# Kernel tuning notes

Measured on AMD Instinct MI355X. Metric: run time of the kernel, lower is better.

The kernel has to match this reference:

```python
import jax, jax.numpy as jnp
import numpy as np

N_NODES = 100000
N_EDGES = 1_600_000


def _glorot(key, shape):
    fan_in, fan_out = shape
    s = jnp.sqrt(6.0 / (fan_in + fan_out)).astype(jnp.float32)
    return jax.random.uniform(key, shape, jnp.float32, -1.0, 1.0) * s


def setup_inputs() -> dict:
    key = jax.random.key(0)
    ks = jax.random.split(key, 6)
    x = jax.random.normal(ks[0], (N_NODES, 88), jnp.float32)
    edge_index = jax.random.randint(ks[1], (2, N_EDGES), 0, N_NODES, dtype=jnp.int32)
    return {
        "x": x,
        "W1": _glorot(ks[2], (88, 65)), "b1": jnp.zeros((65,), jnp.float32),
        "W2": _glorot(ks[3], (65, 50)), "b2": jnp.zeros((50,), jnp.float32),
        "W3": _glorot(ks[4], (50, 65)), "b3": jnp.zeros((65,), jnp.float32),
        "W4": _glorot(ks[5], (65, 88)), "b4": jnp.zeros((88,), jnp.float32),
        "edge_index": edge_index,
    }


def _gcn_conv(h, W, b, src, dst, norm, n):
    # PyG GCNConv: transform, then normalized neighbor aggregation (self-loops
    # already folded into src/dst/norm).
    h = h @ W                                  # [N, out]
    msg = h[src] * norm[:, None]               # [E+N, out] gather
    return jax.ops.segment_sum(msg, dst, num_segments=n) + b  # scatter-add


def reference(x, W1, b1, W2, b2, W3, b3, W4, b4, edge_index):
    n = x.shape[0]
    loop = jnp.arange(n, dtype=edge_index.dtype)
    src = jnp.concatenate([edge_index[0], loop])   # add self-loops
    dst = jnp.concatenate([edge_index[1], loop])
    deg = jax.ops.segment_sum(jnp.ones_like(dst, dtype=x.dtype), dst, num_segments=n)
    dinv = jnp.where(deg > 0, jax.lax.rsqrt(deg), 0.0)
    norm = dinv[src] * dinv[dst]                   # D^-1/2 (A+I) D^-1/2 edge weights

    # encoder
    h = jax.nn.relu(_gcn_conv(x, W1, b1, src, dst, norm, n))
    h = _gcn_conv(h, W2, b2, src, dst, norm, n)
    # decoder
    h = jax.nn.relu(_gcn_conv(h, W3, b3, src, dst, norm, n))
    return _gcn_conv(h, W4, b4, src, dst, norm, n)
```

## Files before the change

kernel.cpp:

```cpp
#include <hip/hip_runtime.h>

#define BS 256
#define FB 1024
#define NB 256
#define CHUNK 4096
#define CAP 64
#define LCAP 8192

using half8 = __attribute__((ext_vector_type(8))) _Float16;

template<typename T>
__device__ __forceinline__ void load8f(const T* p, float (&d)[8]) {
    if constexpr (sizeof(T) == 4) {
        float4 a = *(const float4*)p;
        float4 b = *(const float4*)(p + 4);
        d[0] = a.x; d[1] = a.y; d[2] = a.z; d[3] = a.w;
        d[4] = b.x; d[5] = b.y; d[6] = b.z; d[7] = b.w;
    } else {
        half8 v = *(const half8*)p;
        #pragma unroll
        for (int j = 0; j < 8; ++j) d[j] = (float)v[j];
    }
}
template<typename T>
__device__ __forceinline__ void store8f(T* p, const float (&d)[8]) {
    if constexpr (sizeof(T) == 4) {
        *(float4*)p       = make_float4(d[0], d[1], d[2], d[3]);
        *(float4*)(p + 4) = make_float4(d[4], d[5], d[6], d[7]);
    } else {
        half8 h;
        #pragma unroll
        for (int j = 0; j < 8; ++j) h[j] = (_Float16)d[j];
        *(half8*)p = h;
    }
}


__global__ __launch_bounds__(BS) void k_zero1(int* a, int n) {
    int i = blockIdx.x * BS + threadIdx.x;
    if (i < n) a[i] = 0;
}

__global__ __launch_bounds__(BS) void k_bucket(const int* __restrict__ src, const int* __restrict__ dst,
                                               unsigned* __restrict__ bbuf, int* __restrict__ bcounts,
                                               int E, unsigned long long invB, int bsz) {
    __shared__ int lcnt[NB];
    for (int t = threadIdx.x; t < NB; t += BS) lcnt[t] = 0;
    __syncthreads();
    int base_e = blockIdx.x * CHUNK;
    unsigned* mybuf = bbuf + (size_t)blockIdx.x * NB * CAP;
    #pragma unroll
    for (int j = 0; j < CHUNK / BS; ++j) {
        int e = base_e + j * BS + threadIdx.x;
        if (e < E) {
            int d = dst[e];
            int s = src[e];
            int b = (int)(((unsigned long long)(unsigned)d * invB) >> 40);
            int doff = d - b * bsz;
            int pos = atomicAdd(&lcnt[b], 1);
            if (pos < CAP)
                mybuf[b * CAP + pos] = ((unsigned)doff << 17) | (unsigned)s;
        }
    }
    __syncthreads();
    for (int t = threadIdx.x; t < NB; t += BS)
        bcounts[blockIdx.x * NB + t] = min(lcnt[t], CAP);
}

__global__ __launch_bounds__(FB) void k_cnt(const unsigned* __restrict__ bbuf, const int* __restrict__ bcounts,
                                            int* __restrict__ cnt, int nch, int bsz, int N) {
    __shared__ int lhist[512];
    for (int t = threadIdx.x; t < 512; t += FB) lhist[t] = 0;
    __syncthreads();
    int b = blockIdx.x;
    int lo = b * bsz;
    int total = nch * CAP;
    for (int idx = threadIdx.x; idx < total; idx += FB) {
        int seg = idx >> 6, slot = idx & 63;
        int c = bcounts[seg * NB + b];
        if (slot < c)
            atomicAdd(&lhist[bbuf[((size_t)seg * NB + b) * CAP + slot] >> 17], 1);
    }
    __syncthreads();
    int hi = min(N, lo + bsz);
    for (int t = threadIdx.x; t < hi - lo; t += FB) cnt[lo + t] = lhist[t];
}

__global__ __launch_bounds__(BS) void k_dinv(const int* __restrict__ cnt, float* __restrict__ dinv, int N) {
    int i = blockIdx.x * BS + threadIdx.x;
    if (i < N) dinv[i] = rsqrtf((float)(cnt[i] + 1));
}

__global__ __launch_bounds__(BS) void k_scan1(const int* __restrict__ cnt, int* __restrict__ bsum, int N) {
    __shared__ int s[BS];
    int i = blockIdx.x * BS + threadIdx.x;
    s[threadIdx.x] = (i < N) ? cnt[i] : 0;
    __syncthreads();
    for (int off = BS / 2; off > 0; off >>= 1) {
        if (threadIdx.x < off) s[threadIdx.x] += s[threadIdx.x + off];
        __syncthreads();
    }
    if (threadIdx.x == 0) bsum[blockIdx.x] = s[0];
}

__global__ __launch_bounds__(512) void k_scan2(int* bsum, int nb) {
    __shared__ int s[512];
    int t = threadIdx.x;
    int v = (t < nb) ? bsum[t] : 0;
    s[t] = v;
    __syncthreads();
    for (int off = 1; off < 512; off <<= 1) {
        int u = (t >= off) ? s[t - off] : 0;
        __syncthreads();
        s[t] += u;
        __syncthreads();
    }
    if (t < nb) bsum[t] = s[t] - v;
}

__global__ __launch_bounds__(BS) void k_scan3(const int* __restrict__ cnt, const int* __restrict__ boff,
                                              int* __restrict__ row_ptr, int N) {
    __shared__ int s[BS];
    int t = threadIdx.x;
    int i = blockIdx.x * BS + t;
    int v = (i < N) ? cnt[i] : 0;
    s[t] = v;
    __syncthreads();
    for (int off = 1; off < BS; off <<= 1) {
        int u = (t >= off) ? s[t - off] : 0;
        __syncthreads();
        s[t] += u;
        __syncthreads();
    }
    int base = boff[blockIdx.x];
    if (i < N) row_ptr[i] = base + s[t] - v;
    if (i == N - 1) row_ptr[N] = base + s[t];
}

__global__ __launch_bounds__(FB) void k_fill2(const unsigned* __restrict__ bbuf, const int* __restrict__ bcounts,
                                              const int* __restrict__ row_ptr, const float* __restrict__ dinv,
                                              uint2* __restrict__ entries,
                                              int nch, int bsz, int N) {
    __shared__ int cur[512];
    __shared__ float ldinv[512];
    __shared__ unsigned sorted[LCAP];

    int b = blockIdx.x;
    int lo = b * bsz;
    int hi = min(N, lo + bsz);
    int gbase = row_ptr[lo];
    int tot = row_ptr[hi] - gbase;
    for (int t = threadIdx.x; t < hi - lo; t += FB) {
        cur[t] = row_ptr[lo + t] - gbase;
        ldinv[t] = dinv[lo + t];
    }
    __syncthreads();

    int total = nch * CAP;
    for (int idx = threadIdx.x; idx < total; idx += FB) {
        int seg = idx >> 6, slot = idx & 63;
        int c = bcounts[seg * NB + b];
        if (slot < c) {
            unsigned u = bbuf[((size_t)seg * NB + b) * CAP + slot];
            int p = atomicAdd(&cur[u >> 17], 1);
            if (p < LCAP) sorted[p] = u;
        }
    }
    __syncthreads();

    for (int t = threadIdx.x; t < tot; t += FB) {
        unsigned u = sorted[t];
        int s = (int)(u & 0x1FFFFu);
        int doff = (int)(u >> 17);
        float w = dinv[s] * ldinv[doff];
        entries[gbase + t] = make_uint2((unsigned)s, __float_as_uint(w));
    }
}

template<typename TIN, int K, int M, int LDIN, int LDOUT, bool BIAS, bool RELU, typename TOUT>
__global__ __launch_bounds__(BS) void k_gemm(const TIN* __restrict__ H, const float* __restrict__ Wg,
                                             const float* __restrict__ bias, TOUT* __restrict__ out, int N) {
    constexpr int M8 = (M + 7) & ~7;
    constexpr int MS = M8 + 4;
    constexpr int CG = M8 / 8;
    __shared__ float Wl[K * MS];
    for (int idx = threadIdx.x; idx < K * MS; idx += BS) {
        int k = idx / MS, m = idx - k * MS;
        Wl[idx] = (m < M) ? Wg[(size_t)k * M + m] : 0.f;
    }
    __syncthreads();

    int nrb = (N + 1) >> 1;
    int idx = blockIdx.x * BS + threadIdx.x;
    if (idx >= nrb * CG) return;
    int rb = idx / CG;
    int cg = idx - rb * CG;
    int c0 = cg * 8;
    int r0 = rb * 2;
    bool two = (r0 + 1 < N);
    int r1 = two ? r0 + 1 : r0;
    const TIN* h0 = H + (size_t)r0 * LDIN;
    const TIN* h1 = H + (size_t)r1 * LDIN;

    float acc0[8], acc1[8];
    #pragma unroll
    for (int m = 0; m < 8; ++m) { acc0[m] = 0.f; acc1[m] = 0.f; }

    constexpr int K8 = K & ~7;
    #pragma unroll 1
    for (int k = 0; k < K8; k += 8) {
        float p0[8], p1[8];
        load8f(h0 + k, p0);
        load8f(h1 + k, p1);
        #pragma unroll
        for (int j = 0; j < 8; ++j) {
            const float* wl = &Wl[(k + j) * MS + c0];
            float4 wa = *(const float4*)wl;
            float4 wb = *(const float4*)(wl + 4);
            const float wv[8] = {wa.x, wa.y, wa.z, wa.w, wb.x, wb.y, wb.z, wb.w};
            #pragma unroll
            for (int m = 0; m < 8; ++m) {
                acc0[m] = fmaf(p0[j], wv[m], acc0[m]);
                acc1[m] = fmaf(p1[j], wv[m], acc1[m]);
            }
        }
    }
    #pragma unroll
    for (int k = K8; k < K; ++k) {
        float pa = (float)h0[k];
        float pb = (float)h1[k];
        const float* wl = &Wl[k * MS + c0];
        float4 wa = *(const float4*)wl;
        float4 wb = *(const float4*)(wl + 4);
        const float wv[8] = {wa.x, wa.y, wa.z, wa.w, wb.x, wb.y, wb.z, wb.w};
        #pragma unroll
        for (int m = 0; m < 8; ++m) {
            acc0[m] = fmaf(pa, wv[m], acc0[m]);
            acc1[m] = fmaf(pb, wv[m], acc1[m]);
        }
    }

    #pragma unroll
    for (int m = 0; m < 8; ++m) {
        int c = c0 + m;
        bool in = (c < M);
        float v0 = in ? acc0[m] : 0.f;
        float v1 = in ? acc1[m] : 0.f;
        if (BIAS && in) { float bb = bias[c]; v0 += bb; v1 += bb; }
        if (RELU) { v0 = fmaxf(v0, 0.f); v1 = fmaxf(v1, 0.f); }
        acc0[m] = v0; acc1[m] = v1;
    }
    store8f(out + (size_t)r0 * LDOUT + c0, acc0);
    if (two) store8f(out + (size_t)r1 * LDOUT + c0, acc1);
}

template<typename TIN, typename TOUT, int M, int M8, int LDI, int LDO, bool BIAS, bool RELU>
__global__ __launch_bounds__(BS) void k_agg(const TIN* __restrict__ T, TOUT* __restrict__ out,
                                            const int* __restrict__ row_ptr, const uint2* __restrict__ entries,
                                            const float* __restrict__ dinv, const float* __restrict__ bias,
                                            int N) {
    constexpr int CG = M8 / 8;
    int idx = blockIdx.x * BS + threadIdx.x;
    if (idx >= N * CG) return;
    int i  = idx / CG;
    int cg = idx - i * CG;
    int c0 = cg * 8;

    float di = dinv[i];
    float w0 = di * di;
    float t0[8];
    load8f(T + (size_t)i * LDI + c0, t0);
    float a0[8], a1[8];
    #pragma unroll
    for (int m = 0; m < 8; ++m) { a0[m] = w0 * t0[m]; a1[m] = 0.f; }

    int e0 = row_ptr[i], e1 = row_ptr[i + 1];
    for (int e = e0; e < e1; e += 8) {
        unsigned sidx[8];
        float w[8];
        #pragma unroll
        for (int j = 0; j < 8; ++j) {
            int ee = e + j;
            int ec = (ee < e1) ? ee : (e1 - 1);
            uint2 u = entries[ec];
            sidx[j] = u.x;
            w[j] = (ee < e1) ? __uint_as_float(u.y) : 0.f;
        }
        #pragma unroll
        for (int j = 0; j < 8; ++j) {
            float g[8];
            load8f(T + (size_t)sidx[j] * LDI + c0, g);
            if (j & 1) {
                #pragma unroll
                for (int m = 0; m < 8; ++m) a1[m] = fmaf(w[j], g[m], a1[m]);
            } else {
                #pragma unroll
                for (int m = 0; m < 8; ++m) a0[m] = fmaf(w[j], g[m], a0[m]);
            }
        }
    }

    #pragma unroll
    for (int m = 0; m < 8; ++m) {
        float v = a0[m] + a1[m];
        if (BIAS && (c0 + m) < M) v += bias[c0 + m];
        if (RELU) v = fmaxf(v, 0.f);
        a0[m] = v;
    }
    store8f(out + (size_t)i * LDO + c0, a0);
}


extern "C" void kernel_launch(void* const* d_in, const int* in_sizes, int n_in,
                              void* d_out, int out_size, void* d_ws, size_t ws_size,
                              hipStream_t stream) {
    const float* x  = (const float*)d_in[0];
    const float* W1 = (const float*)d_in[1];
    const float* b1 = (const float*)d_in[2];
    const float* W2 = (const float*)d_in[3];
    const float* b2 = (const float*)d_in[4];
    const float* W3 = (const float*)d_in[5];
    const float* b3 = (const float*)d_in[6];
    const float* W4 = (const float*)d_in[7];
    const float* b4 = (const float*)d_in[8];
    const int* edge_index = (const int*)d_in[9];

    const int N = in_sizes[0] / 88;
    const int E = in_sizes[9] / 2;
    const int* src = edge_index;
    const int* dst = edge_index + E;

    const int nch = (E + CHUNK - 1) / CHUNK;
    const int bsz = (N + NB - 1) / NB;
    const unsigned long long invB = ((1ull << 40) + bsz - 1) / bsz;

    auto al = [](size_t b) { return (b + 255) & ~(size_t)255; };
    char* p = (char*)d_ws;
    auto carve = [&](size_t bytes) { void* r = p; p += (bytes + 255) & ~(size_t)255; return r; };
    int*   cnt     = (int*)  carve((size_t)N * 4);
    float* dinv    = (float*)carve((size_t)N * 4);
    int*   row_ptr = (int*)  carve((size_t)(N + 1) * 4);
    int*   bsum    = (int*)  carve(4096);
    uint2* entries = (uint2*)carve((size_t)E * 8);

    char* ub = p;
    int*      bcounts = (int*)ub;
    unsigned* bbuf    = (unsigned*)(ub + al((size_t)nch * NB * 4));
    size_t csr_bytes  = al((size_t)nch * NB * 4) + al((size_t)nch * NB * CAP * 4);

    size_t hbytes = al((size_t)N * 72 * 2);
    _Float16* hA = (_Float16*)ub;
    _Float16* hB = (_Float16*)(ub + hbytes);
    _Float16* hC = (_Float16*)(ub + 2 * hbytes);
    size_t h_bytes_tot = 3 * hbytes;

    p = ub + (csr_bytes > h_bytes_tot ? csr_bytes : h_bytes_tot);
    (void)p; (void)ws_size;

    int gN = (N + BS - 1) / BS;

    k_zero1 <<<gN, BS, 0, stream>>>(cnt, N);
    k_bucket<<<nch, BS, 0, stream>>>(src, dst, bbuf, bcounts, E, invB, bsz);
    k_cnt   <<<NB, FB, 0, stream>>>(bbuf, bcounts, cnt, nch, bsz, N);
    k_dinv  <<<gN, BS, 0, stream>>>(cnt, dinv, N);
    k_scan1 <<<gN, BS, 0, stream>>>(cnt, bsum, N);
    k_scan2 <<<1, 512, 0, stream>>>(bsum, gN);
    k_scan3 <<<gN, BS, 0, stream>>>(cnt, bsum, row_ptr, N);
    k_fill2 <<<NB, FB, 0, stream>>>(bbuf, bcounts, row_ptr, dinv, entries, nch, bsz, N);

    auto agg_grid  = [&](int CG) { return (N * CG + BS - 1) / BS; };
    auto gemm_grid = [&](int M)  { int M8 = (M + 7) & ~7; int CG = M8 / 8;
                                   return (((N + 1) / 2) * CG + BS - 1) / BS; };

    k_gemm<float, 88, 65, 88, 72, false, false, _Float16><<<gemm_grid(65), BS, 0, stream>>>(x, W1, nullptr, hA, N);
    k_agg<_Float16, _Float16, 65, 72, 72, 72, true, true><<<agg_grid(9), BS, 0, stream>>>(hA, hB, row_ptr, entries, dinv, b1, N);
    k_gemm<_Float16, 65, 50, 72, 56, false, false, _Float16><<<gemm_grid(50), BS, 0, stream>>>(hB, W2, nullptr, hC, N);
    k_agg<_Float16, _Float16, 50, 56, 56, 56, true, false><<<agg_grid(7), BS, 0, stream>>>(hC, hA, row_ptr, entries, dinv, b2, N);
    k_agg<_Float16, _Float16, 50, 56, 56, 56, false, false><<<agg_grid(7), BS, 0, stream>>>(hA, hB, row_ptr, entries, dinv, nullptr, N);
    k_gemm<_Float16, 50, 65, 56, 72, true, true, _Float16><<<gemm_grid(65), BS, 0, stream>>>(hB, W3, b3, hC, N);
    k_agg<_Float16, _Float16, 65, 72, 72, 72, false, false><<<agg_grid(9), BS, 0, stream>>>(hC, hA, row_ptr, entries, dinv, nullptr, N);
    k_gemm<_Float16, 65, 88, 72, 88, true, false, float><<<gemm_grid(88), BS, 0, stream>>>(hA, W4, b4, (float*)d_out, N);
}
```

Measured before the change: 459.4 us.

## Compute four rows per GEMM thread, regroup weights per column group, fuse prep kernels

The GEMM kernel now computes four rows per thread instead of two, and stores the weight matrix in shared memory grouped by 8-column block so each thread reads a contiguous strip. This halves the weight reads from shared memory per output and increases register reuse, but raises register pressure and leaves fewer threads in flight. Separately, the dinv computation is folded into scan1 and the separate zeroing kernel is dropped, which removes two launches. Dropping the zeroing is safe because k_cnt writes every cnt entry.

```diff
diff --git a/kernel.cpp b/kernel.cpp
--- a/kernel.cpp
+++ b/kernel.cpp
@@ -35,11 +35,6 @@
     }
 }
 
-
-__global__ __launch_bounds__(BS) void k_zero1(int* a, int n) {
-    int i = blockIdx.x * BS + threadIdx.x;
-    if (i < n) a[i] = 0;
-}
 
 __global__ __launch_bounds__(BS) void k_bucket(const int* __restrict__ src, const int* __restrict__ dst,
                                                unsigned* __restrict__ bbuf, int* __restrict__ bcounts,
@@ -86,15 +81,13 @@
     for (int t = threadIdx.x; t < hi - lo; t += FB) cnt[lo + t] = lhist[t];
 }
 
-__global__ __launch_bounds__(BS) void k_dinv(const int* __restrict__ cnt, float* __restrict__ dinv, int N) {
-    int i = blockIdx.x * BS + threadIdx.x;
-    if (i < N) dinv[i] = rsqrtf((float)(cnt[i] + 1));
-}
-
-__global__ __launch_bounds__(BS) void k_scan1(const int* __restrict__ cnt, int* __restrict__ bsum, int N) {
+__global__ __launch_bounds__(BS) void k_scan1(const int* __restrict__ cnt, int* __restrict__ bsum,
+                                              float* __restrict__ dinv, int N) {
     __shared__ int s[BS];
     int i = blockIdx.x * BS + threadIdx.x;
-    s[threadIdx.x] = (i < N) ? cnt[i] : 0;
+    int v = (i < N) ? cnt[i] : 0;
+    if (i < N) dinv[i] = rsqrtf((float)(v + 1));
+    s[threadIdx.x] = v;
     __syncthreads();
     for (int off = BS / 2; off > 0; off >>= 1) {
         if (threadIdx.x < off) s[threadIdx.x] += s[threadIdx.x + off];
@@ -181,77 +174,91 @@
 __global__ __launch_bounds__(BS) void k_gemm(const TIN* __restrict__ H, const float* __restrict__ Wg,
                                              const float* __restrict__ bias, TOUT* __restrict__ out, int N) {
     constexpr int M8 = (M + 7) & ~7;
-    constexpr int MS = M8 + 4;
     constexpr int CG = M8 / 8;
-    __shared__ float Wl[K * MS];
-    for (int idx = threadIdx.x; idx < K * MS; idx += BS) {
-        int k = idx / MS, m = idx - k * MS;
-        Wl[idx] = (m < M) ? Wg[(size_t)k * M + m] : 0.f;
-    }
-    __syncthreads();
-
-    int nrb = (N + 1) >> 1;
+    constexpr int WSTR = K * 8 + 4;
+    __shared__ float Wl[CG * WSTR];
+    for (int idx = threadIdx.x; idx < CG * WSTR; idx += BS) {
+        int cg = idx / WSTR, rem = idx - cg * WSTR;
+        int k = rem >> 3, j = rem & 7;
+        int m = cg * 8 + j;
+        Wl[idx] = (rem < K * 8 && m < M) ? Wg[(size_t)k * M + m] : 0.f;
+    }
+    __syncthreads();
+
+    int nrq = (N + 3) >> 2;
     int idx = blockIdx.x * BS + threadIdx.x;
-    if (idx >= nrb * CG) return;
-    int rb = idx / CG;
-    int cg = idx - rb * CG;
+    if (idx >= nrq * CG) return;
+    int rq = idx / CG;
+    int cg = idx - rq * CG;
     int c0 = cg * 8;
-    int r0 = rb * 2;
-    bool two = (r0 + 1 < N);
-    int r1 = two ? r0 + 1 : r0;
-    const TIN* h0 = H + (size_t)r0 * LDIN;
-    const TIN* h1 = H + (size_t)r1 * LDIN;
-
-    float acc0[8], acc1[8];
-    #pragma unroll
-    for (int m = 0; m < 8; ++m) { acc0[m] = 0.f; acc1[m] = 0.f; }
+    int r0 = rq * 4;
+    const float* wb = &Wl[cg * WSTR];
+
+    const TIN* h[4];
+    #pragma unroll
+    for (int r = 0; r < 4; ++r) {
+        int rr = r0 + r; rr = (rr < N) ? rr : (N - 1);
+        h[r] = H + (size_t)rr * LDIN;
+    }
+
+    float acc[4][8];
+    #pragma unroll
+    for (int r = 0; r < 4; ++r)
+        #pragma unroll
+        for (int m = 0; m < 8; ++m) acc[r][m] = 0.f;
 
     constexpr int K8 = K & ~7;
     #pragma unroll 1
     for (int k = 0; k < K8; k += 8) {
-        float p0[8], p1[8];
-        load8f(h0 + k, p0);
-        load8f(h1 + k, p1);
+        float p[4][8];
+        load8f(h[0] + k, p[0]);
+        load8f(h[1] + k, p[1]);
+        load8f(h[2] + k, p[2]);
+        load8f(h[3] + k, p[3]);
+        const float* wl = wb + k * 8;
         #pragma unroll
         for (int j = 0; j < 8; ++j) {
-            const float* wl = &Wl[(k + j) * MS + c0];
-            float4 wa = *(const float4*)wl;
-            float4 wb = *(const float4*)(wl + 4);
-            const float wv[8] = {wa.x, wa.y, wa.z, wa.w, wb.x, wb.y, wb.z, wb.w};
+            float4 wa = *(const float4*)(wl + j * 8);
+            float4 wc = *(const float4*)(wl + j * 8 + 4);
+            const float wv[8] = {wa.x, wa.y, wa.z, wa.w, wc.x, wc.y, wc.z, wc.w};
             #pragma unroll
-            for (int m = 0; m < 8; ++m) {
-                acc0[m] = fmaf(p0[j], wv[m], acc0[m]);
-                acc1[m] = fmaf(p1[j], wv[m], acc1[m]);
-            }
+            for (int r = 0; r < 4; ++r)
+                #pragma unroll
+                for (int m = 0; m < 8; ++m)
+                    acc[r][m] = fmaf(p[r][j], wv[m], acc[r][m]);
         }
     }
     #pragma unroll
     for (int k = K8; k < K; ++k) {
-        float pa = (float)h0[k];
-        float pb = (float)h1[k];
-        const float* wl = &Wl[k * MS + c0];
-        float4 wa = *(const float4*)wl;
-        float4 wb = *(const float4*)(wl + 4);
-        const float wv[8] = {wa.x, wa.y, wa.z, wa.w, wb.x, wb.y, wb.z, wb.w};
+        const float* wl = wb + k * 8;
+        float4 wa = *(const float4*)(wl);
+        float4 wc = *(const float4*)(wl + 4);
+        const float wv[8] = {wa.x, wa.y, wa.z, wa.w, wc.x, wc.y, wc.z, wc.w};
+        #pragma unroll
+        for (int r = 0; r < 4; ++r) {
+            float pv = (float)h[r][k];
+            #pragma unroll
+            for (int m = 0; m < 8; ++m)
+                acc[r][m] = fmaf(pv, wv[m], acc[r][m]);
+        }
+    }
+
+    #pragma unroll
+    for (int r = 0; r < 4; ++r) {
+        int rr = r0 + r;
+        if (rr >= N) break;
+        float v[8];
         #pragma unroll
         for (int m = 0; m < 8; ++m) {
-            acc0[m] = fmaf(pa, wv[m], acc0[m]);
-            acc1[m] = fmaf(pb, wv[m], acc1[m]);
-        }
-    }
-
-    #pragma unroll
-    for (int m = 0; m < 8; ++m) {
-        int c = c0 + m;
-        bool in = (c < M);
-        float v0 = in ? acc0[m] : 0.f;
-        float v1 = in ? acc1[m] : 0.f;
-        if (BIAS && in) { float bb = bias[c]; v0 += bb; v1 += bb; }
-        if (RELU) { v0 = fmaxf(v0, 0.f); v1 = fmaxf(v1, 0.f); }
-        acc0[m] = v0; acc1[m] = v1;
-    }
-    store8f(out + (size_t)r0 * LDOUT + c0, acc0);
-    if (two) store8f(out + (size_t)r1 * LDOUT + c0, acc1);
+            int c = c0 + m;
+            bool in = (c < M);
+            float x = in ? acc[r][m] : 0.f;
+            if (BIAS && in) x += bias[c];
+            if (RELU) x = fmaxf(x, 0.f);
+            v[m] = x;
+        }
+        store8f(out + (size_t)rr * LDOUT + c0, v);
+    }
 }
 
 template<typename TIN, typename TOUT, int M, int M8, int LDI, int LDO, bool BIAS, bool RELU>
@@ -359,18 +366,16 @@
 
     int gN = (N + BS - 1) / BS;
 
-    k_zero1 <<<gN, BS, 0, stream>>>(cnt, N);
     k_bucket<<<nch, BS, 0, stream>>>(src, dst, bbuf, bcounts, E, invB, bsz);
     k_cnt   <<<NB, FB, 0, stream>>>(bbuf, bcounts, cnt, nch, bsz, N);
-    k_dinv  <<<gN, BS, 0, stream>>>(cnt, dinv, N);
-    k_scan1 <<<gN, BS, 0, stream>>>(cnt, bsum, N);
+    k_scan1 <<<gN, BS, 0, stream>>>(cnt, bsum, dinv, N);
     k_scan2 <<<1, 512, 0, stream>>>(bsum, gN);
     k_scan3 <<<gN, BS, 0, stream>>>(cnt, bsum, row_ptr, N);
     k_fill2 <<<NB, FB, 0, stream>>>(bbuf, bcounts, row_ptr, dinv, entries, nch, bsz, N);
 
     auto agg_grid  = [&](int CG) { return (N * CG + BS - 1) / BS; };
     auto gemm_grid = [&](int M)  { int M8 = (M + 7) & ~7; int CG = M8 / 8;
-                                   return (((N + 1) / 2) * CG + BS - 1) / BS; };
+                                   return (((N + 3) / 4) * CG + BS - 1) / BS; };
 
     k_gemm<float, 88, 65, 88, 72, false, false, _Float16><<<gemm_grid(65), BS, 0, stream>>>(x, W1, nullptr, hA, N);
     k_agg<_Float16, _Float16, 65, 72, 72, 72, true, true><<<agg_grid(9), BS, 0, stream>>>(hA, hB, row_ptr, entries, dinv, b1, N);
```

New measurement: 456.0 us. Within noise of the previous version (-0.8%).
